# Kernel tuning notes

Measured on AMD Instinct MI355X. Metric: run time of the kernel, lower is better.

## Reference

```python
import jax, jax.numpy as jnp
import numpy as np

B, N, DIM = 2, 2048, 1024
HEADS, DIM_HEAD = 16, 64
SCALE = DIM_HEAD ** -0.5
MASK_VALUE = -jnp.finfo(jnp.float32).max


def setup_inputs() -> dict:
    key = jax.random.key(0)
    ks = jax.random.split(key, 7)
    inner = HEADS * DIM_HEAD
    x = jax.random.normal(ks[0], (B, N, DIM), dtype=jnp.float32)
    mask = jax.random.randint(ks[1], (B, 1, N, N), 0, 2, dtype=jnp.int32)
    Wq = jax.random.normal(ks[2], (DIM, inner), dtype=jnp.float32) * (DIM ** -0.5)
    Wk = jax.random.normal(ks[3], (DIM, inner), dtype=jnp.float32) * (DIM ** -0.5)
    Wv = jax.random.normal(ks[4], (DIM, inner), dtype=jnp.float32) * (DIM ** -0.5)
    Wo = jax.random.normal(ks[5], (inner, DIM), dtype=jnp.float32) * (inner ** -0.5)
    bo = jnp.zeros((DIM,), dtype=jnp.float32)
    return {"x": x, "mask": mask, "Wq": Wq, "Wk": Wk, "Wv": Wv, "Wo": Wo, "bo": bo}


def reference(x, mask, Wq, Wk, Wv, Wo, bo):
    b, n, _ = x.shape
    # projections -> [b, h, n, d]
    def split_heads(t):
        return t.reshape(b, n, HEADS, DIM_HEAD).transpose(0, 2, 1, 3)
    q = split_heads(x @ Wq)
    k = split_heads(x @ Wk)
    v = split_heads(x @ Wv)
    # full attention scores [b, h, i, j]
    dots = jnp.einsum('bhid,bhjd->bhij', q, k) * SCALE
    # faithful to source: bin_mask = (mask == 0); fill where ~bin_mask
    bin_mask = (mask == 0)
    dots = jnp.where(bin_mask, dots, MASK_VALUE)
    attn = jax.nn.softmax(dots, axis=-1)  # dropout p=0.0 -> identity
    out = jnp.einsum('bhij,bhjd->bhid', attn, v)
    out = out.transpose(0, 2, 1, 3).reshape(b, n, HEADS * DIM_HEAD)
    return out @ Wo + bo
```

## Files before the change

### kernel.cpp

```cpp
#include <hip/hip_runtime.h>
#include <cstdint>
#include <cstddef>

typedef float    f32x4  __attribute__((ext_vector_type(4)));
typedef __bf16   bf16x8 __attribute__((ext_vector_type(8)));
typedef unsigned u32x4  __attribute__((ext_vector_type(4)));
typedef unsigned u32x2  __attribute__((ext_vector_type(2)));
typedef unsigned short u16;
typedef unsigned int   u32;

#define SCL2E 0.18033688011112042f

static __device__ __forceinline__ u16 f2bf(float f) {
    u32 u = __builtin_bit_cast(u32, f);
    u32 r = (u + 0x7FFFu + ((u >> 16) & 1u)) >> 16;
    return (u16)r;
}

static __device__ __forceinline__ u32 cvtpk_bf16(float lo, float hi) {
    u32 r;
    asm("v_cvt_pk_bf16_f32 %0, %1, %2" : "=v"(r) : "v"(lo), "v"(hi));
    return r;
}

static __device__ __forceinline__ float fexp2(float x) {
    float r;
    asm("v_exp_f32 %0, %1" : "=v"(r) : "v"(x));
    return r;
}

static __device__ __forceinline__ void gll16(const u16* g, void* l) {
    __builtin_amdgcn_global_load_lds((const __attribute__((address_space(1))) void*)g,
                                     (__attribute__((address_space(3))) void*)l, 16, 0, 0);
}

static __device__ __forceinline__ void bar() {
    asm volatile("s_barrier" ::: "memory");
}


__global__ __launch_bounds__(256) void prep_k(
    const float* __restrict__ x, u16* __restrict__ xb,
    const float* __restrict__ W0, const float* __restrict__ W1,
    const float* __restrict__ W2, const float* __restrict__ W3,
    u16* __restrict__ T0, u16* __restrict__ T1,
    u16* __restrict__ T2, u16* __restrict__ T3,
    const int* __restrict__ mask, u32* __restrict__ mp)
{
    __shared__ float T[64][65];
    const int bid = blockIdx.x;
    if (bid < 2048) {
        const long i = ((long)bid * 256 + threadIdx.x) * 8;
        f32x4 a = *(const f32x4*)(x + i);
        f32x4 c = *(const f32x4*)(x + i + 4);
        u32x4 o;
        o[0] = (u32)f2bf(a[0]) | ((u32)f2bf(a[1]) << 16);
        o[1] = (u32)f2bf(a[2]) | ((u32)f2bf(a[3]) << 16);
        o[2] = (u32)f2bf(c[0]) | ((u32)f2bf(c[1]) << 16);
        o[3] = (u32)f2bf(c[2]) | ((u32)f2bf(c[3]) << 16);
        *(u32x4*)(xb + i) = o;
    } else if (bid < 3072) {
        const int idx = bid - 2048;
        const int z = idx >> 8, rem = idx & 255;
        const int n0 = (rem & 15) * 64, k0 = (rem >> 4) * 64;
        const float* W = (z == 0) ? W0 : (z == 1) ? W1 : (z == 2) ? W2 : W3;
        u16* Wt = (z == 0) ? T0 : (z == 1) ? T1 : (z == 2) ? T2 : T3;
        const float scl = (z == 0) ? SCL2E : 1.0f;
        const int c = threadIdx.x & 63, r0 = (threadIdx.x >> 6) * 16;
#pragma unroll
        for (int i = 0; i < 16; ++i)
            T[r0 + i][c] = W[(long)(k0 + r0 + i) * 1024 + n0 + c];
        __syncthreads();
#pragma unroll
        for (int i = 0; i < 16; ++i)
            Wt[(long)(n0 + r0 + i) * 1024 + k0 + c] = f2bf(T[c][r0 + i] * scl);
    } else {
        const long wi = (long)(bid - 3072) * 256 + threadIdx.x;
        const int* src = mask + wi * 32;
        u32 word = 0;
#pragma unroll
        for (int c = 0; c < 8; ++c) {
            const int4 v = *(const int4*)(src + c * 4);
            word |= (u32)(v.x != 0) << (c * 4);
            word |= (u32)(v.y != 0) << (c * 4 + 1);
            word |= (u32)(v.z != 0) << (c * 4 + 2);
            word |= (u32)(v.w != 0) << (c * 4 + 3);
        }
        mp[wi] = word;
    }
}

__global__ __launch_bounds__(256) void vt_k(const u16* __restrict__ v, u16* __restrict__ vt) {
    __shared__ u16 T[64][66];
    const int nt = blockIdx.x, h = blockIdx.y, b = blockIdx.z;
    const int c = threadIdx.x & 63, r0 = (threadIdx.x >> 6) * 16;
    const u16* src = v + ((long)b * 2048 + nt * 64) * 1024 + h * 64;
    u16* dst = vt + ((long)(b * 16 + h) * 64) * 2048 + nt * 64;
#pragma unroll
    for (int i = 0; i < 16; ++i)
        T[r0 + i][c] = src[(long)(r0 + i) * 1024 + c];
    __syncthreads();
#pragma unroll
    for (int i = 0; i < 16; ++i)
        dst[(long)(r0 + i) * 2048 + c] = T[c][r0 + i];
}


__global__ __launch_bounds__(512, 2) void gemm_qkv(
    const u16* __restrict__ Ag, const u16* __restrict__ Btg, u16* __restrict__ C0)
{
    __shared__ u16 Asm[2][256 * 64];
    __shared__ u16 Bsm[2][256 * 64];

    const int tid = threadIdx.x, lane = tid & 63, w = tid >> 6;
    const int wm = w >> 2, wn = w & 3;
    const int g = lane >> 4, lr = lane & 15;

    const int L = blockIdx.x;
    const int xcd = L & 7, idx = L >> 3;
    const long mBase = (long)((xcd & 3) * 4 + (idx & 3)) * 256;
    const long nBase = (long)((xcd >> 2) * 6 + (idx >> 2)) * 256;

    const int srow = tid >> 3;
    const int scolb = ((tid & 7) << 4) ^ ((srow & 7) << 4);
    const long aoff = (mBase + srow) * 1024 + (scolb >> 1);
    const long boff = (nBase + srow) * 1024 + (scolb >> 1);
    const int ldst = tid * 16;

    int kb[2];
#pragma unroll
    for (int ks = 0; ks < 2; ++ks) kb[ks] = (ks * 64 + g * 16) ^ ((lr & 7) << 4);

    auto stA = [&](int d, int h, int kt) {
        gll16(Ag + aoff + (long)h * 131072 + (long)kt * 64,
              (char*)&Asm[d][0] + h * 16384 + ldst);
        gll16(Ag + aoff + (long)h * 131072 + 65536 + (long)kt * 64,
              (char*)&Asm[d][0] + h * 16384 + 8192 + ldst);
    };
    auto stB = [&](int d, int h, int kt) {
        gll16(Btg + boff + (long)h * 131072 + (long)kt * 64,
              (char*)&Bsm[d][0] + h * 16384 + ldst);
        gll16(Btg + boff + (long)h * 131072 + 65536 + (long)kt * 64,
              (char*)&Bsm[d][0] + h * 16384 + 8192 + ldst);
    };
    auto rdA = [&](int d, int mi, int ks) {
        return *(const bf16x8*)((const char*)&Asm[d][0] + (wm * 128 + mi * 16 + lr) * 128 + kb[ks]);
    };
    auto rdB = [&](int d, int ni, int ks) {
        return *(const bf16x8*)((const char*)&Bsm[d][0] + (wn * 64 + ni * 16 + lr) * 128 + kb[ks]);
    };

    f32x4 acc[8][4];
#pragma unroll
    for (int i = 0; i < 8; ++i)
#pragma unroll
        for (int j = 0; j < 4; ++j) acc[i][j] = f32x4{0.f, 0.f, 0.f, 0.f};

    stB(0, 0, 0); stB(0, 1, 0);
    stA(0, 0, 0); stA(0, 1, 0);
    stB(1, 0, 1); stB(1, 1, 1);
    asm volatile("s_waitcnt vmcnt(4)" ::: "memory");
    bar();

    auto ktile = [&](int d, int ktA, int ktB, bool doA, bool doB, int vm) {
        bf16x8 af[4][2], bfr[4][2];
#pragma unroll
        for (int mi = 0; mi < 4; ++mi) {
            af[mi][0] = rdA(d, mi, 0);
            af[mi][1] = rdA(d, mi, 1);
        }
#pragma unroll
        for (int ni = 0; ni < 2; ++ni) {
            bfr[ni][0] = rdB(d, ni, 0);
            bfr[ni][1] = rdB(d, ni, 1);
        }
        if (doA) stA(d ^ 1, 0, ktA);
        bar();
        __builtin_amdgcn_s_setprio(1);
#pragma unroll
        for (int mi = 0; mi < 4; ++mi)
#pragma unroll
            for (int ni = 0; ni < 2; ++ni) {
                acc[mi][ni] = __builtin_amdgcn_mfma_f32_16x16x32_bf16(af[mi][0], bfr[ni][0], acc[mi][ni], 0, 0, 0);
                acc[mi][ni] = __builtin_amdgcn_mfma_f32_16x16x32_bf16(af[mi][1], bfr[ni][1], acc[mi][ni], 0, 0, 0);
            }
        __builtin_amdgcn_s_setprio(0);
        bar();
#pragma unroll
        for (int ni = 2; ni < 4; ++ni) {
            bfr[ni][0] = rdB(d, ni, 0);
            bfr[ni][1] = rdB(d, ni, 1);
        }
        if (doA) stA(d ^ 1, 1, ktA);
        bar();
        __builtin_amdgcn_s_setprio(1);
#pragma unroll
        for (int mi = 0; mi < 4; ++mi)
#pragma unroll
            for (int ni = 2; ni < 4; ++ni) {
                acc[mi][ni] = __builtin_amdgcn_mfma_f32_16x16x32_bf16(af[mi][0], bfr[ni][0], acc[mi][ni], 0, 0, 0);
                acc[mi][ni] = __builtin_amdgcn_mfma_f32_16x16x32_bf16(af[mi][1], bfr[ni][1], acc[mi][ni], 0, 0, 0);
            }
        __builtin_amdgcn_s_setprio(0);
        bar();
#pragma unroll
        for (int mi = 0; mi < 4; ++mi) {
            af[mi][0] = rdA(d, mi + 4, 0);
            af[mi][1] = rdA(d, mi + 4, 1);
        }
        if (doB) stB(d, 0, ktB);
        bar();
        __builtin_amdgcn_s_setprio(1);
#pragma unroll
        for (int mi = 0; mi < 4; ++mi)
#pragma unroll
            for (int ni = 0; ni < 2; ++ni) {
                acc[mi + 4][ni] = __builtin_amdgcn_mfma_f32_16x16x32_bf16(af[mi][0], bfr[ni][0], acc[mi + 4][ni], 0, 0, 0);
                acc[mi + 4][ni] = __builtin_amdgcn_mfma_f32_16x16x32_bf16(af[mi][1], bfr[ni][1], acc[mi + 4][ni], 0, 0, 0);
            }
        __builtin_amdgcn_s_setprio(0);
        bar();
        if (doB) stB(d, 1, ktB);
        bar();
        __builtin_amdgcn_s_setprio(1);
#pragma unroll
        for (int mi = 0; mi < 4; ++mi)
#pragma unroll
            for (int ni = 2; ni < 4; ++ni) {
                acc[mi + 4][ni] = __builtin_amdgcn_mfma_f32_16x16x32_bf16(af[mi][0], bfr[ni][0], acc[mi + 4][ni], 0, 0, 0);
                acc[mi + 4][ni] = __builtin_amdgcn_mfma_f32_16x16x32_bf16(af[mi][1], bfr[ni][1], acc[mi + 4][ni], 0, 0, 0);
            }
        __builtin_amdgcn_s_setprio(0);
        if (vm == 0)      asm volatile("s_waitcnt vmcnt(4)" ::: "memory");
        else if (vm == 1) asm volatile("s_waitcnt vmcnt(0)" ::: "memory");
        bar();
    };

    for (int c = 0; c < 14; c += 2) {
        ktile(0, c + 1, c + 2, true, true, 0);
        ktile(1, c + 2, c + 3, true, true, 0);
    }
    ktile(0, 15, 16, true, false, 1);
    ktile(1, 16, 17, false, false, 2);

    const int wsel = (int)(nBase >> 10);
    u16* Cw = C0 + (long)wsel * (4096l * 1024);
    const long ncl = (nBase & 1023) + wn * 64;
    const long rbase = mBase + wm * 128;
#pragma unroll
    for (int mi = 0; mi < 8; ++mi)
#pragma unroll
        for (int r = 0; r < 4; ++r) {
            const long row = rbase + mi * 16 + g * 4 + r;
#pragma unroll
            for (int ni = 0; ni < 4; ++ni)
                Cw[row * 1024 + ncl + ni * 16 + lr] = f2bf(acc[mi][ni][r]);
        }
}


__global__ __launch_bounds__(256, 2) void gemm_out(
    const u16* __restrict__ A, const u16* __restrict__ Bt,
    float* __restrict__ Cf, const float* __restrict__ bias)
{
    constexpr int K = 1024, N = 1024;
    __shared__ u16 As[2][64 * 32];
    __shared__ u16 Bs[2][128 * 32];
    const int tid = threadIdx.x;
    const int wave = tid >> 6, lane = tid & 63;
    const int wr = wave >> 1, wc = wave & 1;
    const int g = lane >> 4, lr = lane & 15;
    const long mBase = (long)blockIdx.y * 64;
    const long nBase = (long)blockIdx.x * 128;

    f32x4 acc[2][4];
#pragma unroll
    for (int i = 0; i < 2; ++i)
#pragma unroll
        for (int j = 0; j < 4; ++j) acc[i][j] = f32x4{0.f, 0.f, 0.f, 0.f};

    const int oA = tid * 16;
    const int rA = oA >> 6, cbA = oA & 63;
    const int o0 = tid * 16, o1 = (256 + tid) * 16;
    const int r0 = o0 >> 6, cb0 = o0 & 63;
    const int r1 = o1 >> 6, cb1 = o1 & 63;

    gll16(A  + (mBase + rA) * K + (cbA >> 1), (char*)&As[0][0] + oA);
    gll16(Bt + (nBase + r0) * K + (cb0 >> 1), (char*)&Bs[0][0] + o0);
    gll16(Bt + (nBase + r1) * K + (cb1 >> 1), (char*)&Bs[0][0] + o1);
    __syncthreads();

#pragma unroll 2
    for (int kt = 0; kt < 32; ++kt) {
        const int buf = kt & 1;
        if (kt + 1 < 32) {
            const long ko = (long)(kt + 1) * 32;
            gll16(A  + (mBase + rA) * K + ko + (cbA >> 1), (char*)&As[buf ^ 1][0] + oA);
            gll16(Bt + (nBase + r0) * K + ko + (cb0 >> 1), (char*)&Bs[buf ^ 1][0] + o0);
            gll16(Bt + (nBase + r1) * K + ko + (cb1 >> 1), (char*)&Bs[buf ^ 1][0] + o1);
        }
        bf16x8 af[2], bfv[4];
#pragma unroll
        for (int mi = 0; mi < 2; ++mi)
            af[mi] = *(const bf16x8*)((const char*)&As[buf][0] + (wr * 32 + mi * 16 + lr) * 64 + g * 16);
#pragma unroll
        for (int ni = 0; ni < 4; ++ni)
            bfv[ni] = *(const bf16x8*)((const char*)&Bs[buf][0] + (wc * 64 + ni * 16 + lr) * 64 + g * 16);
#pragma unroll
        for (int mi = 0; mi < 2; ++mi)
#pragma unroll
            for (int ni = 0; ni < 4; ++ni)
                acc[mi][ni] = __builtin_amdgcn_mfma_f32_16x16x32_bf16(af[mi], bfv[ni], acc[mi][ni], 0, 0, 0);
        __syncthreads();
    }

#pragma unroll
    for (int mi = 0; mi < 2; ++mi)
#pragma unroll
        for (int r = 0; r < 4; ++r) {
            const long row = mBase + wr * 32 + mi * 16 + g * 4 + r;
#pragma unroll
            for (int ni = 0; ni < 4; ++ni) {
                const long col = nBase + wc * 64 + ni * 16 + lr;
                Cf[row * N + col] = acc[mi][ni][r] + bias[col];
            }
        }
}


__global__ __launch_bounds__(512, 2) void attn_fwd(
    const u16* __restrict__ Qg_, const u16* __restrict__ Kg_, const u16* __restrict__ Vtg_,
    const u32* __restrict__ maskp, u16* __restrict__ Og_)
{
    __shared__ u16 Ks[2][2][64 * 64];
    __shared__ u16 Vs[2][2][64 * 64];

    const int tid = threadIdx.x, w = tid >> 6, lane = tid & 63;
    const int g = lane >> 4, lr = lane & 15;
    const int L = blockIdx.x;
    const int slot = L >> 3;
    const int grp = (L & 7) + 8 * (slot >> 3);
    const int q0 = (slot & 7) * 256;
    const int b = grp >> 4, h = grp & 15;
    const u16* Qg = Qg_ + ((long)b * 2048) * 1024 + h * 64;
    const u16* Kg = Kg_ + ((long)b * 2048) * 1024 + h * 64;
    const u16* Vtg = Vtg_ + ((long)grp * 64) * 2048;
    u16* Og = Og_ + ((long)b * 2048) * 1024 + h * 64;

    const int ldso = tid * 16;
    const int m = ldso >> 7, cb = ldso & 127;
    const int sb = cb ^ ((m & 7) << 4);
    const int kap = ((m >> 4) & 1) * 32 + ((m >> 2) & 3) * 8 + ((m >> 5) & 1) * 4 + (m & 3);
    const long ksrc = (long)kap * 1024 + (sb >> 1);
    const long vsrc = (long)m * 2048 + (sb >> 1);

    bf16x8 qf[2][2];
#pragma unroll
    for (int nq = 0; nq < 2; ++nq)
#pragma unroll
        for (int ks = 0; ks < 2; ++ks)
            qf[nq][ks] = *(const bf16x8*)(Qg + (long)(q0 + w * 32 + nq * 16 + lr) * 1024 + ks * 32 + g * 8);

    const long mrow0 = (long)b * 2048 + q0 + w * 32 + lr;
    const u32* mpr0 = maskp + mrow0 * 64;
    const u32* mpr1 = maskp + (mrow0 + 16) * 64;

    u32x4 mwC0 = *(const u32x4*)(mpr0);
    u32x4 mwC1 = *(const u32x4*)(mpr1);
#pragma unroll
    for (int hh = 0; hh < 2; ++hh) {
        gll16(Kg + hh * 65536 + ksrc, (char*)&Ks[0][hh][0] + ldso);
        gll16(Vtg + hh * 64 + vsrc, (char*)&Vs[0][hh][0] + ldso);
    }
    __syncthreads();

    const int swz = (lr & 7) << 4;
    int kb[2];
#pragma unroll
    for (int ks = 0; ks < 2; ++ks) kb[ks] = (ks * 64 + g * 16) ^ swz;

    f32x4 oacc[2][4];
#pragma unroll
    for (int i = 0; i < 2; ++i)
#pragma unroll
        for (int j = 0; j < 4; ++j) oacc[i][j] = f32x4{0.f, 0.f, 0.f, 0.f};
    f32x4 osum[2];
    osum[0] = f32x4{0.f, 0.f, 0.f, 0.f};
    osum[1] = f32x4{0.f, 0.f, 0.f, 0.f};
    const f32x4 z4 = {0.f, 0.f, 0.f, 0.f};
    const u32x4 ones4 = {0x3F803F80u, 0x3F803F80u, 0x3F803F80u, 0x3F803F80u};
    const bf16x8 ones8 = __builtin_bit_cast(bf16x8, ones4);

#pragma unroll 2
    for (int t = 0; t < 16; ++t) {
        const int cur = t & 1;
        u32x4 mwN0, mwN1;
        if (t + 1 < 16) {
            mwN0 = *(const u32x4*)(mpr0 + (t + 1) * 4);
            mwN1 = *(const u32x4*)(mpr1 + (t + 1) * 4);
            const long kv0 = (long)(t + 1) * 128;
#pragma unroll
            for (int hh = 0; hh < 2; ++hh) {
                gll16(Kg + (kv0 + hh * 64) * 1024 + ksrc, (char*)&Ks[cur ^ 1][hh][0] + ldso);
                gll16(Vtg + kv0 + hh * 64 + vsrc, (char*)&Vs[cur ^ 1][hh][0] + ldso);
            }
        }

#pragma unroll
        for (int hh = 0; hh < 2; ++hh) {
            const char* kbase = (const char*)&Ks[cur][hh][0];
            const char* vbase = (const char*)&Vs[cur][hh][0];

            f32x4 s[4][2];
            __builtin_amdgcn_s_setprio(1);
#pragma unroll
            for (int mt = 0; mt < 4; ++mt) {
                const bf16x8 kf0 = *(const bf16x8*)(kbase + (mt * 16 + lr) * 128 + kb[0]);
                const bf16x8 kf1 = *(const bf16x8*)(kbase + (mt * 16 + lr) * 128 + kb[1]);
#pragma unroll
                for (int nq = 0; nq < 2; ++nq) {
                    s[mt][nq] = __builtin_amdgcn_mfma_f32_16x16x32_bf16(kf0, qf[nq][0], z4, 0, 0, 0);
                    s[mt][nq] = __builtin_amdgcn_mfma_f32_16x16x32_bf16(kf1, qf[nq][1], s[mt][nq], 0, 0, 0);
                }
            }
            __builtin_amdgcn_s_setprio(0);

            u32 pk[4][2][2];
#pragma unroll
            for (int ts = 0; ts < 4; ++ts) {
                const int sh = g * 8 + (ts >> 1) * 4;
                const int wi = hh * 2 + (ts & 1);
#pragma unroll
                for (int nq = 0; nq < 2; ++nq) {
                    const u32 word = nq ? mwC1[wi] : mwC0[wi];
                    const u32 iwsh = (~word) >> sh;
                    float e[4];
#pragma unroll
                    for (int r = 0; r < 4; ++r) {
                        const float ev = fexp2(s[ts][nq][r]);
                        const u32 keep = (u32)__builtin_amdgcn_sbfe((int)iwsh, (u32)r, 1u);
                        e[r] = __builtin_bit_cast(float, __builtin_bit_cast(u32, ev) & keep);
                    }
                    pk[ts][nq][0] = cvtpk_bf16(e[0], e[1]);
                    pk[ts][nq][1] = cvtpk_bf16(e[2], e[3]);
                }
            }

            bf16x8 pa[2][2];
#pragma unroll
            for (int nq = 0; nq < 2; ++nq)
#pragma unroll
                for (int ks = 0; ks < 2; ++ks) {
                    u32x4 t4;
                    t4[0] = pk[ks][nq][0]; t4[1] = pk[ks][nq][1];
                    t4[2] = pk[ks + 2][nq][0]; t4[3] = pk[ks + 2][nq][1];
                    pa[nq][ks] = __builtin_bit_cast(bf16x8, t4);
                }
            __builtin_amdgcn_s_setprio(1);
#pragma unroll
            for (int nq = 0; nq < 2; ++nq)
#pragma unroll
                for (int ks = 0; ks < 2; ++ks)
                    osum[nq] = __builtin_amdgcn_mfma_f32_16x16x32_bf16(pa[nq][ks], ones8, osum[nq], 0, 0, 0);
#pragma unroll
            for (int dt = 0; dt < 4; ++dt)
#pragma unroll
                for (int ks = 0; ks < 2; ++ks) {
                    const bf16x8 vf = *(const bf16x8*)(vbase + (dt * 16 + lr) * 128 + kb[ks]);
#pragma unroll
                    for (int nq = 0; nq < 2; ++nq)
                        oacc[nq][dt] = __builtin_amdgcn_mfma_f32_16x16x32_bf16(pa[nq][ks], vf, oacc[nq][dt], 0, 0, 0);
                }
            __builtin_amdgcn_s_setprio(0);
        }
        __syncthreads();

        mwC0 = mwN0; mwC1 = mwN1;
    }

#pragma unroll
    for (int nq = 0; nq < 2; ++nq)
#pragma unroll
        for (int rr = 0; rr < 4; ++rr) {
            const float inv = __builtin_amdgcn_rcpf(osum[nq][rr]);
            const long row = (long)q0 + w * 32 + nq * 16 + g * 4 + rr;
#pragma unroll
            for (int dt = 0; dt < 4; ++dt)
                Og[row * 1024 + dt * 16 + lr] = f2bf(oacc[nq][dt][rr] * inv);
        }
}


extern "C" void kernel_launch(void* const* d_in, const int* in_sizes, int n_in,
                              void* d_out, int out_size, void* d_ws, size_t ws_size,
                              hipStream_t stream)
{
    (void)in_sizes; (void)n_in; (void)out_size; (void)ws_size;
    const float* x    = (const float*)d_in[0];
    const int*   mask = (const int*)d_in[1];
    const float* Wq   = (const float*)d_in[2];
    const float* Wk   = (const float*)d_in[3];
    const float* Wv   = (const float*)d_in[4];
    const float* Wo   = (const float*)d_in[5];
    const float* bo   = (const float*)d_in[6];
    float* out = (float*)d_out;

    char* ws = (char*)d_ws;
    u16* xb    = (u16*)(ws);
    u16* vtws  = (u16*)(ws);
    u16* WqT   = (u16*)(ws + (8l  << 20));
    u16* WkT   = (u16*)(ws + (10l << 20));
    u16* WvT   = (u16*)(ws + (12l << 20));
    u16* WoT   = (u16*)(ws + (14l << 20));
    u16* qws   = (u16*)(ws + (16l << 20));
    u16* kws   = (u16*)(ws + (24l << 20));
    u16* vws   = (u16*)(ws + (32l << 20));
    u16* inner = (u16*)(ws + (40l << 20));
    u32* mp    = (u32*)(ws + (48l << 20));

    prep_k<<<4096, 256, 0, stream>>>(x, xb, Wq, Wk, Wv, Wo, WqT, WkT, WvT, WoT, mask, mp);
    gemm_qkv<<<192, 512, 0, stream>>>(xb, WqT, qws);
    vt_k<<<dim3(32, 16, 2), 256, 0, stream>>>(vws, vtws);
    attn_fwd<<<256, 512, 0, stream>>>(qws, kws, vtws, mp, inner);
    gemm_out<<<dim3(8, 64), 256, 0, stream>>>(inner, WoT, out, bo);
}
```

Measured before the change: 128.3 us.

## Fuse V transpose into QKV GEMM by computing V^T directly; batch QK MFMAs

```diff
diff --git a/kernel.cpp b/kernel.cpp
--- a/kernel.cpp
+++ b/kernel.cpp
@@ -90,24 +90,10 @@
     }
 }
 
-__global__ __launch_bounds__(256) void vt_k(const u16* __restrict__ v, u16* __restrict__ vt) {
-    __shared__ u16 T[64][66];
-    const int nt = blockIdx.x, h = blockIdx.y, b = blockIdx.z;
-    const int c = threadIdx.x & 63, r0 = (threadIdx.x >> 6) * 16;
-    const u16* src = v + ((long)b * 2048 + nt * 64) * 1024 + h * 64;
-    u16* dst = vt + ((long)(b * 16 + h) * 64) * 2048 + nt * 64;
-#pragma unroll
-    for (int i = 0; i < 16; ++i)
-        T[r0 + i][c] = src[(long)(r0 + i) * 1024 + c];
-    __syncthreads();
-#pragma unroll
-    for (int i = 0; i < 16; ++i)
-        dst[(long)(r0 + i) * 2048 + c] = T[c][r0 + i];
-}
-
 
 __global__ __launch_bounds__(512, 2) void gemm_qkv(
-    const u16* __restrict__ Ag, const u16* __restrict__ Btg, u16* __restrict__ C0)
+    const u16* __restrict__ Ag, const u16* __restrict__ Btg,
+    u16* __restrict__ C0, u16* __restrict__ Vt)
 {
     __shared__ u16 Asm[2][256 * 64];
     __shared__ u16 Bsm[2][256 * 64];
@@ -120,6 +106,7 @@
     const int xcd = L & 7, idx = L >> 3;
     const long mBase = (long)((xcd & 3) * 4 + (idx & 3)) * 256;
     const long nBase = (long)((xcd >> 2) * 6 + (idx >> 2)) * 256;
+    const bool vblk = (nBase >= 2048);
 
     const int srow = tid >> 3;
     const int scolb = ((tid & 7) << 4) ^ ((srow & 7) << 4);
@@ -127,20 +114,25 @@
     const long boff = (nBase + srow) * 1024 + (scolb >> 1);
     const int ldst = tid * 16;
 
+    const u16* AsrcP = vblk ? Btg : Ag;
+    const u16* BsrcP = vblk ? Ag  : Btg;
+    const long aoffE = vblk ? boff : aoff;
+    const long boffE = vblk ? aoff : boff;
+
     int kb[2];
 #pragma unroll
     for (int ks = 0; ks < 2; ++ks) kb[ks] = (ks * 64 + g * 16) ^ ((lr & 7) << 4);
 
     auto stA = [&](int d, int h, int kt) {
-        gll16(Ag + aoff + (long)h * 131072 + (long)kt * 64,
+        gll16(AsrcP + aoffE + (long)h * 131072 + (long)kt * 64,
               (char*)&Asm[d][0] + h * 16384 + ldst);
-        gll16(Ag + aoff + (long)h * 131072 + 65536 + (long)kt * 64,
+        gll16(AsrcP + aoffE + (long)h * 131072 + 65536 + (long)kt * 64,
               (char*)&Asm[d][0] + h * 16384 + 8192 + ldst);
     };
     auto stB = [&](int d, int h, int kt) {
-        gll16(Btg + boff + (long)h * 131072 + (long)kt * 64,
+        gll16(BsrcP + boffE + (long)h * 131072 + (long)kt * 64,
               (char*)&Bsm[d][0] + h * 16384 + ldst);
-        gll16(Btg + boff + (long)h * 131072 + 65536 + (long)kt * 64,
+        gll16(BsrcP + boffE + (long)h * 131072 + 65536 + (long)kt * 64,
               (char*)&Bsm[d][0] + h * 16384 + 8192 + ldst);
     };
     auto rdA = [&](int d, int mi, int ks) {
@@ -243,19 +235,34 @@
     ktile(0, 15, 16, true, false, 1);
     ktile(1, 16, 17, false, false, 2);
 
-    const int wsel = (int)(nBase >> 10);
-    u16* Cw = C0 + (long)wsel * (4096l * 1024);
-    const long ncl = (nBase & 1023) + wn * 64;
-    const long rbase = mBase + wm * 128;
-#pragma unroll
-    for (int mi = 0; mi < 8; ++mi)
-#pragma unroll
-        for (int r = 0; r < 4; ++r) {
-            const long row = rbase + mi * 16 + g * 4 + r;
-#pragma unroll
-            for (int ni = 0; ni < 4; ++ni)
-                Cw[row * 1024 + ncl + ni * 16 + lr] = f2bf(acc[mi][ni][r]);
-        }
+    if (!vblk) {
+        const int wsel = (int)(nBase >> 10);
+        u16* Cw = C0 + (long)wsel * (4096l * 1024);
+        const long ncl = (nBase & 1023) + wn * 64;
+        const long rbase = mBase + wm * 128;
+#pragma unroll
+        for (int mi = 0; mi < 8; ++mi)
+#pragma unroll
+            for (int r = 0; r < 4; ++r) {
+                const long row = rbase + mi * 16 + g * 4 + r;
+#pragma unroll
+                for (int ni = 0; ni < 4; ++ni)
+                    Cw[row * 1024 + ncl + ni * 16 + lr] = f2bf(acc[mi][ni][r]);
+            }
+    } else {
+        const long nb = nBase - 2048;
+#pragma unroll
+        for (int mi = 0; mi < 8; ++mi)
+#pragma unroll
+            for (int r = 0; r < 4; ++r) {
+                const long rowN = nb + wm * 128 + mi * 16 + g * 4 + r;
+#pragma unroll
+                for (int ni = 0; ni < 4; ++ni) {
+                    const long colT = mBase + wn * 64 + ni * 16 + lr;
+                    Vt[rowN * 4096 + colT] = f2bf(acc[mi][ni][r]);
+                }
+            }
+    }
 }
 
 
@@ -344,7 +351,7 @@
     const int b = grp >> 4, h = grp & 15;
     const u16* Qg = Qg_ + ((long)b * 2048) * 1024 + h * 64;
     const u16* Kg = Kg_ + ((long)b * 2048) * 1024 + h * 64;
-    const u16* Vtg = Vtg_ + ((long)grp * 64) * 2048;
+    const u16* Vtg = Vtg_ + (long)(h * 64) * 4096 + (long)b * 2048;
     u16* Og = Og_ + ((long)b * 2048) * 1024 + h * 64;
 
     const int ldso = tid * 16;
@@ -352,7 +359,7 @@
     const int sb = cb ^ ((m & 7) << 4);
     const int kap = ((m >> 4) & 1) * 32 + ((m >> 2) & 3) * 8 + ((m >> 5) & 1) * 4 + (m & 3);
     const long ksrc = (long)kap * 1024 + (sb >> 1);
-    const long vsrc = (long)m * 2048 + (sb >> 1);
+    const long vsrc = (long)m * 4096 + (sb >> 1);
 
     bf16x8 qf[2][2];
 #pragma unroll
@@ -406,24 +413,27 @@
             }
         }
 
+        f32x4 s2[2][4][2];
+        __builtin_amdgcn_s_setprio(1);
 #pragma unroll
         for (int hh = 0; hh < 2; ++hh) {
             const char* kbase = (const char*)&Ks[cur][hh][0];
-            const char* vbase = (const char*)&Vs[cur][hh][0];
-
-            f32x4 s[4][2];
-            __builtin_amdgcn_s_setprio(1);
 #pragma unroll
             for (int mt = 0; mt < 4; ++mt) {
                 const bf16x8 kf0 = *(const bf16x8*)(kbase + (mt * 16 + lr) * 128 + kb[0]);
                 const bf16x8 kf1 = *(const bf16x8*)(kbase + (mt * 16 + lr) * 128 + kb[1]);
 #pragma unroll
                 for (int nq = 0; nq < 2; ++nq) {
-                    s[mt][nq] = __builtin_amdgcn_mfma_f32_16x16x32_bf16(kf0, qf[nq][0], z4, 0, 0, 0);
-                    s[mt][nq] = __builtin_amdgcn_mfma_f32_16x16x32_bf16(kf1, qf[nq][1], s[mt][nq], 0, 0, 0);
+                    s2[hh][mt][nq] = __builtin_amdgcn_mfma_f32_16x16x32_bf16(kf0, qf[nq][0], z4, 0, 0, 0);
+                    s2[hh][mt][nq] = __builtin_amdgcn_mfma_f32_16x16x32_bf16(kf1, qf[nq][1], s2[hh][mt][nq], 0, 0, 0);
                 }
             }
-            __builtin_amdgcn_s_setprio(0);
+        }
+        __builtin_amdgcn_s_setprio(0);
+
+#pragma unroll
+        for (int hh = 0; hh < 2; ++hh) {
+            const char* vbase = (const char*)&Vs[cur][hh][0];
 
             u32 pk[4][2][2];
 #pragma unroll
@@ -437,7 +447,7 @@
                     float e[4];
 #pragma unroll
                     for (int r = 0; r < 4; ++r) {
-                        const float ev = fexp2(s[ts][nq][r]);
+                        const float ev = fexp2(s2[hh][ts][nq][r]);
                         const u32 keep = (u32)__builtin_amdgcn_sbfe((int)iwsh, (u32)r, 1u);
                         e[r] = __builtin_bit_cast(float, __builtin_bit_cast(u32, ev) & keep);
                     }
@@ -507,20 +517,19 @@
 
     char* ws = (char*)d_ws;
     u16* xb    = (u16*)(ws);
-    u16* vtws  = (u16*)(ws);
     u16* WqT   = (u16*)(ws + (8l  << 20));
     u16* WkT   = (u16*)(ws + (10l << 20));
     u16* WvT   = (u16*)(ws + (12l << 20));
     u16* WoT   = (u16*)(ws + (14l << 20));
     u16* qws   = (u16*)(ws + (16l << 20));
     u16* kws   = (u16*)(ws + (24l << 20));
-    u16* vws   = (u16*)(ws + (32l << 20));
+    u16* vtws  = (u16*)(ws + (32l << 20));
     u16* inner = (u16*)(ws + (40l << 20));
     u32* mp    = (u32*)(ws + (48l << 20));
 
     prep_k<<<4096, 256, 0, stream>>>(x, xb, Wq, Wk, Wv, Wo, WqT, WkT, WvT, WoT, mask, mp);
-    gemm_qkv<<<192, 512, 0, stream>>>(xb, WqT, qws);
-    vt_k<<<dim3(32, 16, 2), 256, 0, stream>>>(vws, vtws);
+    gemm_qkv<<<192, 512, 0, stream>>>(xb, WqT, qws, vtws);
     attn_fwd<<<256, 512, 0, stream>>>(qws, kws, vtws, mp, inner);
     gemm_out<<<dim3(8, 64), 256, 0, stream>>>(inner, WoT, out, bo);
-}
+    (void)kws;
+}
```

Measured after the change: 124.7 us. 2.8% less time.
